# Kernel tuning notes

Measured on AMD Instinct MI355X. Metric: run time of the kernel, lower is better.

## Reference

```python
import jax, jax.numpy as jnp
import numpy as np

N_NODES = 100000
N_EDGES = 1600000
NUM_GRAPHS = 128
F_IN = 64
HID = 64


def setup_inputs() -> dict:
    key = jax.random.key(0)
    ks = jax.random.split(key, 10)
    x = jax.random.normal(ks[0], (N_NODES, F_IN), dtype=jnp.float32)
    edge_index = jax.random.randint(ks[1], (2, N_EDGES), 0, N_NODES, dtype=jnp.int64)
    batch = jnp.sort(jax.random.randint(ks[2], (N_NODES,), 0, NUM_GRAPHS, dtype=jnp.int64))
    def glorot(k, shape):
        lim = float(np.sqrt(6.0 / (shape[0] + shape[1])))
        return jax.random.uniform(k, shape, dtype=jnp.float32, minval=-lim, maxval=lim)
    return {
        "x": x,
        "edge_index": edge_index,
        "batch": batch,
        "W1": glorot(ks[3], (F_IN, HID)), "b1": jnp.zeros((HID,), jnp.float32),
        "W2": glorot(ks[4], (HID, HID)), "b2": jnp.zeros((HID,), jnp.float32),
        "W3": glorot(ks[5], (HID, HID)), "b3": jnp.zeros((HID,), jnp.float32),
        "fc1_w": glorot(ks[6], (HID, 10)), "fc1_b": jnp.zeros((10,), jnp.float32),
        "fc2_w": glorot(ks[7], (10, 1)), "fc2_b": jnp.zeros((1,), jnp.float32),
    }


def reference(x, edge_index, batch, W1, b1, W2, b2, W3, b3, fc1_w, fc1_b, fc2_w, fc2_b):
    n = x.shape[0]
    # GCN normalization with self-loops (PyG gcn_norm): deg over dst incl. self-loop
    loop = jnp.arange(n, dtype=edge_index.dtype)
    src = jnp.concatenate([edge_index[0], loop])
    dst = jnp.concatenate([edge_index[1], loop])
    deg = jax.ops.segment_sum(jnp.ones_like(dst, dtype=x.dtype), dst, num_segments=n)
    dinv = jnp.where(deg > 0, jax.lax.rsqrt(deg), 0.0)
    norm = (dinv[src] * dinv[dst])[:, None]  # [E+N, 1]

    def gcn_conv(h, W, b):
        h = h @ W                      # dense linear transform
        msg = h[src] * norm            # gather + degree normalize
        agg = jax.ops.segment_sum(msg, dst, num_segments=n)  # scatter-add
        return agg + b

    h = jax.nn.relu(gcn_conv(x, W1, b1))
    h = jax.nn.relu(gcn_conv(h, W2, b2))
    h = jax.nn.relu(gcn_conv(h, W3, b3))

    # global mean pool over graphs
    sums = jax.ops.segment_sum(h, batch, num_segments=NUM_GRAPHS)
    counts = jax.ops.segment_sum(jnp.ones((n,), h.dtype), batch, num_segments=NUM_GRAPHS)
    pooled = sums / jnp.maximum(counts, 1.0)[:, None]  # [NUM_GRAPHS, HID]

    out = jax.nn.relu(pooled @ fc1_w + fc1_b)
    return out @ fc2_w + fc2_b  # [NUM_GRAPHS, 1]
```

## Files before the change

### kernel.cpp

```cpp
#include <hip/hip_runtime.h>
#include <hip/hip_fp16.h>

#define N_NODES   100000
#define N_EDGES   1600000
#define NUM_GRAPHS 128
#define HID       64

#define NB   512
#define NPB  196
#define NBU  511
#define CPE  3125
#define CSR_TOT (N_EDGES + N_NODES)


__global__ void k_zero(int* __restrict__ p, int n) {
  int i = blockIdx.x * blockDim.x + threadIdx.x;
  if (i < n) p[i] = 0;
}

__global__ void k_f2h(const float* __restrict__ in, __half* __restrict__ out, int n4) {
  int i = blockIdx.x * blockDim.x + threadIdx.x;
  if (i >= n4) return;
  float4 v = ((const float4*)in)[i];
  ((__half2*)out)[2 * i]     = __floats2half2_rn(v.x, v.y);
  ((__half2*)out)[2 * i + 1] = __floats2half2_rn(v.z, v.w);
}

__global__ __launch_bounds__(256) void k_b1a(const int* __restrict__ dst, int* __restrict__ H) {
  __shared__ int hist[NB];
  int w = blockIdx.x, t = threadIdx.x;
  for (int b = t; b < NB; b += 256) hist[b] = 0;
  __syncthreads();
  int e0 = w * CPE;
  for (int i = t; i < CPE; i += 256)
    atomicAdd(&hist[dst[e0 + i] / NPB], 1);
  __syncthreads();
  for (int b = t; b < NB; b += 256) H[w * NB + b] = hist[b];
}

__global__ __launch_bounds__(256) void k_colsum(const int* __restrict__ H, int* __restrict__ S) {
  __shared__ int red[256];
  int b = blockIdx.x, t = threadIdx.x;
  red[t] = H[t * NB + b] + H[(t + 256) * NB + b];
  __syncthreads();
  for (int d = 128; d > 0; d >>= 1) { if (t < d) red[t] += red[t + d]; __syncthreads(); }
  if (t == 0) S[b] = red[0];
}

__global__ __launch_bounds__(512) void k_rowscan(const int* __restrict__ H,
                                                 const int* __restrict__ S,
                                                 int* __restrict__ bstart,
                                                 int* __restrict__ OT) {
  __shared__ int sb[NB];
  __shared__ int sc[NB];
  int b = blockIdx.x, t = threadIdx.x;
  int sv = S[t];
  sb[t] = sv; __syncthreads();
  for (int d = 1; d < NB; d <<= 1) {
    int x = (t >= d) ? sb[t - d] : 0; __syncthreads();
    sb[t] += x; __syncthreads();
  }
  int bst = sb[b] - S[b];
  if (t == 0) bstart[b] = bst;
  if (b == NB - 1 && t == 0) bstart[NB] = sb[NB - 1];
  int v = H[t * NB + b];
  sc[t] = v; __syncthreads();
  for (int d = 1; d < NB; d <<= 1) {
    int x = (t >= d) ? sc[t - d] : 0; __syncthreads();
    sc[t] += x; __syncthreads();
  }
  OT[b * NB + t] = bst + sc[t] - v;
}

__global__ __launch_bounds__(256) void k_b1b(const int* __restrict__ src,
                                             const int* __restrict__ dst,
                                             const int* __restrict__ OT,
                                             int2* __restrict__ staged) {
  __shared__ int pos[NB];
  int w = blockIdx.x, t = threadIdx.x;
  for (int b = t; b < NB; b += 256) pos[b] = OT[b * NB + w];
  __syncthreads();
  int e0 = w * CPE;
  for (int i = t; i < CPE; i += 256) {
    int s = src[e0 + i], d = dst[e0 + i];
    int p = atomicAdd(&pos[d / NPB], 1);
    staged[p] = make_int2(s, d);
  }
}

__global__ __launch_bounds__(256) void k_b2a(const int2* __restrict__ staged,
                                             const int* __restrict__ bstart,
                                             int* __restrict__ row_off,
                                             float* __restrict__ dinv) {
  __shared__ int cnt[256];
  __shared__ int sc[256];
  int b = blockIdx.x, t = threadIdx.x;
  int nloc = min(NPB, N_NODES - b * NPB);
  cnt[t] = 0;
  __syncthreads();
  int s0 = bstart[b], s1 = bstart[b + 1];
  for (int i = s0 + t; i < s1; i += 256)
    atomicAdd(&cnt[staged[i].y - b * NPB], 1);
  __syncthreads();
  int v = (t < nloc) ? cnt[t] + 1 : 0;
  sc[t] = v; __syncthreads();
  for (int d = 1; d < 256; d <<= 1) {
    int x = (t >= d) ? sc[t - d] : 0; __syncthreads();
    sc[t] += x; __syncthreads();
  }
  if (t < nloc) {
    int g = b * NPB + t;
    row_off[g] = bstart[b] + b * NPB + (sc[t] - v);
    dinv[g] = rsqrtf((float)(cnt[t] + 1));
  }
  if (b == 0 && t == 0) row_off[N_NODES] = CSR_TOT;
}

__global__ __launch_bounds__(256) void k_b2b(const int2* __restrict__ staged,
                                             const int* __restrict__ bstart,
                                             const int* __restrict__ row_off,
                                             const float* __restrict__ dinv,
                                             int2* __restrict__ csr) {
  __shared__ int pos[NPB];
  __shared__ float dl[NPB];
  int b = blockIdx.x, t = threadIdx.x;
  int nloc = min(NPB, N_NODES - b * NPB);
  if (t < nloc) {
    int g = b * NPB + t;
    int ro = row_off[g];
    float dv = dinv[g];
    csr[ro] = make_int2(g, __float_as_int(dv * dv));
    pos[t] = ro + 1;
    dl[t] = dv;
  }
  __syncthreads();
  int s0 = bstart[b], s1 = bstart[b + 1];
  for (int i = s0 + t; i < s1; i += 256) {
    int2 e = staged[i];
    int l = e.y - b * NPB;
    int p = atomicAdd(&pos[l], 1);
    csr[p] = make_int2(e.x, __float_as_int(dl[l] * dinv[e.x]));
  }
}


__global__ __launch_bounds__(256) void k_gemm(const __half* __restrict__ A,
                                              const float* __restrict__ W,
                                              __half* __restrict__ C) {
  __shared__ float sW[64 * 64];
  __shared__ float sA[64][65];
  int tid = threadIdx.x;
  #pragma unroll
  for (int i = tid; i < 1024; i += 256)
    ((float4*)sW)[i] = ((const float4*)W)[i];
  int row0 = blockIdx.x * 64;
  #pragma unroll
  for (int i = tid; i < 1024; i += 256) {
    int r = i >> 4, c4 = (i & 15) << 2;
    int row = row0 + r;
    if (row < N_NODES) {
      __half2 a = *(const __half2*)(A + (size_t)row * 64 + c4);
      __half2 b = *(const __half2*)(A + (size_t)row * 64 + c4 + 2);
      float2 fa = __half22float2(a), fb = __half22float2(b);
      sA[r][c4 + 0] = fa.x; sA[r][c4 + 1] = fa.y;
      sA[r][c4 + 2] = fb.x; sA[r][c4 + 3] = fb.y;
    } else {
      sA[r][c4 + 0] = 0.f; sA[r][c4 + 1] = 0.f; sA[r][c4 + 2] = 0.f; sA[r][c4 + 3] = 0.f;
    }
  }
  __syncthreads();
  int tr = (tid >> 4) << 2;
  int tc = (tid & 15) << 2;
  float acc[4][4];
  #pragma unroll
  for (int i = 0; i < 4; ++i)
    #pragma unroll
    for (int j = 0; j < 4; ++j) acc[i][j] = 0.f;
  #pragma unroll 8
  for (int k = 0; k < 64; ++k) {
    float4 w = *(const float4*)&sW[k * 64 + tc];
    float a0 = sA[tr + 0][k], a1 = sA[tr + 1][k], a2 = sA[tr + 2][k], a3 = sA[tr + 3][k];
    acc[0][0] += a0 * w.x; acc[0][1] += a0 * w.y; acc[0][2] += a0 * w.z; acc[0][3] += a0 * w.w;
    acc[1][0] += a1 * w.x; acc[1][1] += a1 * w.y; acc[1][2] += a1 * w.z; acc[1][3] += a1 * w.w;
    acc[2][0] += a2 * w.x; acc[2][1] += a2 * w.y; acc[2][2] += a2 * w.z; acc[2][3] += a2 * w.w;
    acc[3][0] += a3 * w.x; acc[3][1] += a3 * w.y; acc[3][2] += a3 * w.z; acc[3][3] += a3 * w.w;
  }
  #pragma unroll
  for (int i = 0; i < 4; ++i) {
    int row = row0 + tr + i;
    if (row < N_NODES) {
      *(__half2*)(C + (size_t)row * 64 + tc)     = __floats2half2_rn(acc[i][0], acc[i][1]);
      *(__half2*)(C + (size_t)row * 64 + tc + 2) = __floats2half2_rn(acc[i][2], acc[i][3]);
    }
  }
}


__global__ __launch_bounds__(256) void k_agg(const __half2* __restrict__ hw2,
                                             const int* __restrict__ row_off,
                                             const int2* __restrict__ csr,
                                             const float2* __restrict__ bias2,
                                             __half2* __restrict__ out2) {
  int tid = threadIdx.x;
  int half_id = tid >> 5;
  int f = tid & 31;
  int v = blockIdx.x * 8 + half_id;
  if (v >= N_NODES) return;
  int o = row_off[v], e = row_off[v + 1];
  float accx = 0.f, accy = 0.f;
  int i = o;
  for (; i + 4 <= e; i += 4) {
    int2 p0 = csr[i + 0];
    int2 p1 = csr[i + 1];
    int2 p2 = csr[i + 2];
    int2 p3 = csr[i + 3];
    float2 h0 = __half22float2(hw2[(size_t)p0.x * 32 + f]);
    float2 h1 = __half22float2(hw2[(size_t)p1.x * 32 + f]);
    float2 h2 = __half22float2(hw2[(size_t)p2.x * 32 + f]);
    float2 h3 = __half22float2(hw2[(size_t)p3.x * 32 + f]);
    float n0 = __int_as_float(p0.y), n1 = __int_as_float(p1.y);
    float n2 = __int_as_float(p2.y), n3 = __int_as_float(p3.y);
    accx += n0 * h0.x; accy += n0 * h0.y;
    accx += n1 * h1.x; accy += n1 * h1.y;
    accx += n2 * h2.x; accy += n2 * h2.y;
    accx += n3 * h3.x; accy += n3 * h3.y;
  }
  for (; i < e; ++i) {
    int2 p = csr[i];
    float2 h = __half22float2(hw2[(size_t)p.x * 32 + f]);
    float n = __int_as_float(p.y);
    accx += n * h.x; accy += n * h.y;
  }
  float2 b = bias2[f];
  out2[(size_t)v * 32 + f] =
      __floats2half2_rn(fmaxf(accx + b.x, 0.f), fmaxf(accy + b.y, 0.f));
}


#define POOL_CHUNK 32

__global__ __launch_bounds__(256) void k_pool(const __half* __restrict__ h,
                                              const int* __restrict__ batch,
                                              float* __restrict__ pooled,
                                              int* __restrict__ pcnt) {
  int wid = threadIdx.x >> 6, lane = threadIdx.x & 63;
  int w = blockIdx.x * (blockDim.x >> 6) + wid;
  int v0 = w * POOL_CHUNK;
  if (v0 >= N_NODES) return;
  int vend = min(v0 + POOL_CHUNK, N_NODES);
  int g = batch[v0];
  float acc = 0.0f;
  int cnt = 0;
  for (int v = v0; v < vend; ++v) {
    int gv = batch[v];
    if (gv != g) {
      atomicAdd(&pooled[g * HID + lane], acc);
      if (lane == 0) atomicAdd(&pcnt[g], cnt);
      g = gv; acc = 0.0f; cnt = 0;
    }
    acc += __half2float(h[(size_t)v * HID + lane]);
    ++cnt;
  }
  atomicAdd(&pooled[g * HID + lane], acc);
  if (lane == 0) atomicAdd(&pcnt[g], cnt);
}

__global__ void k_mlp(const float* __restrict__ pooled, const int* __restrict__ pcnt,
                      const float* __restrict__ fc1w, const float* __restrict__ fc1b,
                      const float* __restrict__ fc2w, const float* __restrict__ fc2b,
                      float* __restrict__ out) {
  int g = threadIdx.x;
  if (g >= NUM_GRAPHS) return;
  float inv = 1.0f / fmaxf((float)pcnt[g], 1.0f);
  float hid[10];
  #pragma unroll
  for (int j = 0; j < 10; ++j) hid[j] = fc1b[j];
  for (int k = 0; k < HID; ++k) {
    float p = pooled[g * HID + k] * inv;
    #pragma unroll
    for (int j = 0; j < 10; ++j) hid[j] += p * fc1w[k * 10 + j];
  }
  float o = fc2b[0];
  #pragma unroll
  for (int j = 0; j < 10; ++j) o += fmaxf(hid[j], 0.0f) * fc2w[j];
  out[g] = o;
}


extern "C" void kernel_launch(void* const* d_in, const int* in_sizes, int n_in,
                              void* d_out, int out_size, void* d_ws, size_t ws_size,
                              hipStream_t stream) {
  const float* x    = (const float*)d_in[0];
  const int*   ei   = (const int*)d_in[1];
  const int*   batch= (const int*)d_in[2];
  const float* W1   = (const float*)d_in[3];
  const float* b1   = (const float*)d_in[4];
  const float* W2   = (const float*)d_in[5];
  const float* b2   = (const float*)d_in[6];
  const float* W3   = (const float*)d_in[7];
  const float* b3   = (const float*)d_in[8];
  const float* fc1w = (const float*)d_in[9];
  const float* fc1b = (const float*)d_in[10];
  const float* fc2w = (const float*)d_in[11];
  const float* fc2b = (const float*)d_in[12];

  const int* e_src = ei;
  const int* e_dst = ei + N_EDGES;

  char* ws = (char*)d_ws;
  auto alignup = [](size_t o, size_t a) { return (o + a - 1) / a * a; };
  size_t off = 0;
  int*   H      = (int*)(ws + off);  off += (size_t)NB * NB * 4;
  int*   pcnt   = (int*)(ws + off);  off += 128 * 4;
  float* pooled = (float*)(ws + off); off += 8192 * 4;
  const int ZERO_N = NB * NB + 128 + 8192;
  int*   S      = (int*)(ws + off);  off += NB * 4;
  int*   bstart = (int*)(ws + off);  off += (NB + 1) * 4;  off = alignup(off, 256);
  int*   OT     = (int*)(ws + off);  off += (size_t)NB * NB * 4;          off = alignup(off, 256);
  int*   row_off= (int*)(ws + off);  off += (size_t)(N_NODES + 1) * 4;    off = alignup(off, 256);
  float* dinv   = (float*)(ws + off); off += (size_t)N_NODES * 4;         off = alignup(off, 256);
  int2*  csr    = (int2*)(ws + off); off += (size_t)CSR_TOT * 8;          off = alignup(off, 256);
  __half* xh    = (__half*)(ws + off); off += (size_t)N_NODES * HID * 2;  off = alignup(off, 256);
  __half* h_a   = (__half*)(ws + off); off += (size_t)N_NODES * HID * 2;  off = alignup(off, 256);
  int2*  staged = (int2*)(ws + off);
  __half* h_b   = (__half*)(ws + off); off += (size_t)N_EDGES * 8;
  (void)ws_size; (void)in_sizes; (void)n_in; (void)out_size;

  const int TB = 256;
  k_zero   <<<(ZERO_N + TB - 1) / TB, TB, 0, stream>>>(H, ZERO_N);
  k_f2h    <<<(N_NODES * HID / 4 + TB - 1) / TB, TB, 0, stream>>>(x, xh, N_NODES * HID / 4);
  k_b1a    <<<NB, TB, 0, stream>>>(e_dst, H);
  k_colsum <<<NB, TB, 0, stream>>>(H, S);
  k_rowscan<<<NB, 512, 0, stream>>>(H, S, bstart, OT);
  k_b1b    <<<NB, TB, 0, stream>>>(e_src, e_dst, OT, staged);
  k_b2a    <<<NBU, TB, 0, stream>>>(staged, bstart, row_off, dinv);
  k_b2b    <<<NBU, TB, 0, stream>>>(staged, bstart, row_off, dinv, csr);

  const int GEMM_GRID = (N_NODES + 63) / 64;
  const int AGG_GRID  = (N_NODES + 7) / 8;

  k_gemm<<<GEMM_GRID, TB, 0, stream>>>(xh, W1, h_a);
  k_agg <<<AGG_GRID, TB, 0, stream>>>((const __half2*)h_a, row_off, csr,
                                      (const float2*)b1, (__half2*)h_b);
  k_gemm<<<GEMM_GRID, TB, 0, stream>>>(h_b, W2, h_a);
  k_agg <<<AGG_GRID, TB, 0, stream>>>((const __half2*)h_a, row_off, csr,
                                      (const float2*)b2, (__half2*)h_b);
  k_gemm<<<GEMM_GRID, TB, 0, stream>>>(h_b, W3, h_a);
  k_agg <<<AGG_GRID, TB, 0, stream>>>((const __half2*)h_a, row_off, csr,
                                      (const float2*)b3, (__half2*)h_b);

  const int POOL_GRID = ((N_NODES + POOL_CHUNK - 1) / POOL_CHUNK + 3) / 4;
  k_pool<<<POOL_GRID, TB, 0, stream>>>(h_b, batch, pooled, pcnt);
  k_mlp <<<1, 128, 0, stream>>>(pooled, pcnt, fc1w, fc1b, fc2w, fc2b, (float*)d_out);
}
```

Baseline: 287.7 us.

## Sort nodes by degree and aggregate with 8 lanes per node using 16-byte loads

```diff
diff --git a/kernel.cpp b/kernel.cpp
--- a/kernel.cpp
+++ b/kernel.cpp
@@ -144,6 +144,55 @@
 }
 
 
+__global__ __launch_bounds__(256) void k_dhist(const int* __restrict__ row_off,
+                                               int* __restrict__ dbins) {
+  __shared__ int h[256];
+  int t = threadIdx.x;
+  h[t] = 0;
+  __syncthreads();
+  int v = blockIdx.x * 256 + t;
+  if (v < N_NODES) {
+    int deg = min(row_off[v + 1] - row_off[v], 255);
+    atomicAdd(&h[deg], 1);
+  }
+  __syncthreads();
+  if (h[t] > 0) atomicAdd(&dbins[t], h[t]);
+}
+
+__global__ __launch_bounds__(256) void k_dscan(const int* __restrict__ dbins,
+                                               int* __restrict__ dpos) {
+  __shared__ int sc[256];
+  int t = threadIdx.x;
+  int v = dbins[t];
+  sc[t] = v; __syncthreads();
+  for (int d = 1; d < 256; d <<= 1) {
+    int x = (t >= d) ? sc[t - d] : 0; __syncthreads();
+    sc[t] += x; __syncthreads();
+  }
+  dpos[t] = sc[t] - v;
+}
+
+__global__ __launch_bounds__(256) void k_dperm(const int* __restrict__ row_off,
+                                               int* __restrict__ dpos,
+                                               int* __restrict__ perm) {
+  __shared__ int cnt[256];
+  __shared__ int sbase[256];
+  int t = threadIdx.x;
+  cnt[t] = 0;
+  __syncthreads();
+  int v = blockIdx.x * 256 + t;
+  int bin = 0, rank = 0;
+  if (v < N_NODES) {
+    bin = min(row_off[v + 1] - row_off[v], 255);
+    rank = atomicAdd(&cnt[bin], 1);
+  }
+  __syncthreads();
+  if (cnt[t] > 0) sbase[t] = atomicAdd(&dpos[t], cnt[t]);
+  __syncthreads();
+  if (v < N_NODES) perm[sbase[bin] + rank] = v;
+}
+
+
 __global__ __launch_bounds__(256) void k_gemm(const __half* __restrict__ A,
                                               const float* __restrict__ W,
                                               __half* __restrict__ C) {
@@ -196,44 +245,80 @@
 }
 
 
-__global__ __launch_bounds__(256) void k_agg(const __half2* __restrict__ hw2,
+__device__ __forceinline__ void fma8(float* acc, float n, uint4 h) {
+  __half2 u0 = *(__half2*)&h.x, u1 = *(__half2*)&h.y;
+  __half2 u2 = *(__half2*)&h.z, u3 = *(__half2*)&h.w;
+  float2 f0 = __half22float2(u0), f1 = __half22float2(u1);
+  float2 f2 = __half22float2(u2), f3 = __half22float2(u3);
+  acc[0] = fmaf(n, f0.x, acc[0]); acc[1] = fmaf(n, f0.y, acc[1]);
+  acc[2] = fmaf(n, f1.x, acc[2]); acc[3] = fmaf(n, f1.y, acc[3]);
+  acc[4] = fmaf(n, f2.x, acc[4]); acc[5] = fmaf(n, f2.y, acc[5]);
+  acc[6] = fmaf(n, f3.x, acc[6]); acc[7] = fmaf(n, f3.y, acc[7]);
+}
+
+__global__ __launch_bounds__(256) void k_agg(const __half* __restrict__ hw,
                                              const int* __restrict__ row_off,
                                              const int2* __restrict__ csr,
-                                             const float2* __restrict__ bias2,
-                                             __half2* __restrict__ out2) {
+                                             const int* __restrict__ perm,
+                                             const float* __restrict__ bias,
+                                             __half* __restrict__ out) {
   int tid = threadIdx.x;
-  int half_id = tid >> 5;
-  int f = tid & 31;
-  int v = blockIdx.x * 8 + half_id;
-  if (v >= N_NODES) return;
-  int o = row_off[v], e = row_off[v + 1];
-  float accx = 0.f, accy = 0.f;
-  int i = o;
-  for (; i + 4 <= e; i += 4) {
-    int2 p0 = csr[i + 0];
-    int2 p1 = csr[i + 1];
-    int2 p2 = csr[i + 2];
-    int2 p3 = csr[i + 3];
-    float2 h0 = __half22float2(hw2[(size_t)p0.x * 32 + f]);
-    float2 h1 = __half22float2(hw2[(size_t)p1.x * 32 + f]);
-    float2 h2 = __half22float2(hw2[(size_t)p2.x * 32 + f]);
-    float2 h3 = __half22float2(hw2[(size_t)p3.x * 32 + f]);
-    float n0 = __int_as_float(p0.y), n1 = __int_as_float(p1.y);
-    float n2 = __int_as_float(p2.y), n3 = __int_as_float(p3.y);
-    accx += n0 * h0.x; accy += n0 * h0.y;
-    accx += n1 * h1.x; accy += n1 * h1.y;
-    accx += n2 * h2.x; accy += n2 * h2.y;
-    accx += n3 * h3.x; accy += n3 * h3.y;
-  }
-  for (; i < e; ++i) {
-    int2 p = csr[i];
-    float2 h = __half22float2(hw2[(size_t)p.x * 32 + f]);
-    float n = __int_as_float(p.y);
-    accx += n * h.x; accy += n * h.y;
-  }
-  float2 b = bias2[f];
-  out2[(size_t)v * 32 + f] =
-      __floats2half2_rn(fmaxf(accx + b.x, 0.f), fmaxf(accy + b.y, 0.f));
+  int lane = tid & 63;
+  int sg = lane >> 3;
+  int k = lane & 7;
+  int slot = (blockIdx.x * 4 + (tid >> 6)) * 8 + sg;
+  int v = -1, o = 0, d = 1;
+  if (slot < N_NODES) {
+    v = perm[slot];
+    o = row_off[v];
+    d = row_off[v + 1] - o;
+  }
+  int m = d;
+  m = max(m, __shfl_xor(m, 8));
+  m = max(m, __shfl_xor(m, 16));
+  m = max(m, __shfl_xor(m, 32));
+  float acc[8];
+  #pragma unroll
+  for (int j = 0; j < 8; ++j) acc[j] = 0.f;
+  const __half* hk = hw + k * 8;
+  int dm1 = d - 1;
+  int i = 0;
+  for (; i + 4 <= m; i += 4) {
+    int2 p0 = csr[o + min(i + 0, dm1)];
+    int2 p1 = csr[o + min(i + 1, dm1)];
+    int2 p2 = csr[o + min(i + 2, dm1)];
+    int2 p3 = csr[o + min(i + 3, dm1)];
+    uint4 h0 = *(const uint4*)(hk + (size_t)p0.x * 64);
+    uint4 h1 = *(const uint4*)(hk + (size_t)p1.x * 64);
+    uint4 h2 = *(const uint4*)(hk + (size_t)p2.x * 64);
+    uint4 h3 = *(const uint4*)(hk + (size_t)p3.x * 64);
+    float n0 = (i + 0 < d) ? __int_as_float(p0.y) : 0.f;
+    float n1 = (i + 1 < d) ? __int_as_float(p1.y) : 0.f;
+    float n2 = (i + 2 < d) ? __int_as_float(p2.y) : 0.f;
+    float n3 = (i + 3 < d) ? __int_as_float(p3.y) : 0.f;
+    fma8(acc, n0, h0);
+    fma8(acc, n1, h1);
+    fma8(acc, n2, h2);
+    fma8(acc, n3, h3);
+  }
+  for (; i < m; ++i) {
+    int2 p = csr[o + min(i, dm1)];
+    uint4 h = *(const uint4*)(hk + (size_t)p.x * 64);
+    float n = (i < d) ? __int_as_float(p.y) : 0.f;
+    fma8(acc, n, h);
+  }
+  if (v >= 0) {
+    float4 b0 = *(const float4*)(bias + k * 8);
+    float4 b1 = *(const float4*)(bias + k * 8 + 4);
+    __half2 q0 = __floats2half2_rn(fmaxf(acc[0] + b0.x, 0.f), fmaxf(acc[1] + b0.y, 0.f));
+    __half2 q1 = __floats2half2_rn(fmaxf(acc[2] + b0.z, 0.f), fmaxf(acc[3] + b0.w, 0.f));
+    __half2 q2 = __floats2half2_rn(fmaxf(acc[4] + b1.x, 0.f), fmaxf(acc[5] + b1.y, 0.f));
+    __half2 q3 = __floats2half2_rn(fmaxf(acc[6] + b1.z, 0.f), fmaxf(acc[7] + b1.w, 0.f));
+    uint4 r;
+    r.x = *(unsigned int*)&q0; r.y = *(unsigned int*)&q1;
+    r.z = *(unsigned int*)&q2; r.w = *(unsigned int*)&q3;
+    *(uint4*)(out + (size_t)v * HID + k * 8) = r;
+  }
 }
 
 
@@ -313,12 +398,15 @@
   int*   H      = (int*)(ws + off);  off += (size_t)NB * NB * 4;
   int*   pcnt   = (int*)(ws + off);  off += 128 * 4;
   float* pooled = (float*)(ws + off); off += 8192 * 4;
-  const int ZERO_N = NB * NB + 128 + 8192;
+  int*   dbins  = (int*)(ws + off);  off += 256 * 4;
+  const int ZERO_N = NB * NB + 128 + 8192 + 256;
   int*   S      = (int*)(ws + off);  off += NB * 4;
-  int*   bstart = (int*)(ws + off);  off += (NB + 1) * 4;  off = alignup(off, 256);
+  int*   bstart = (int*)(ws + off);  off += (NB + 1) * 4;
+  int*   dpos   = (int*)(ws + off);  off += 256 * 4;       off = alignup(off, 256);
   int*   OT     = (int*)(ws + off);  off += (size_t)NB * NB * 4;          off = alignup(off, 256);
   int*   row_off= (int*)(ws + off);  off += (size_t)(N_NODES + 1) * 4;    off = alignup(off, 256);
   float* dinv   = (float*)(ws + off); off += (size_t)N_NODES * 4;         off = alignup(off, 256);
+  int*   perm   = (int*)(ws + off);  off += (size_t)N_NODES * 4;          off = alignup(off, 256);
   int2*  csr    = (int2*)(ws + off); off += (size_t)CSR_TOT * 8;          off = alignup(off, 256);
   __half* xh    = (__half*)(ws + off); off += (size_t)N_NODES * HID * 2;  off = alignup(off, 256);
   __half* h_a   = (__half*)(ws + off); off += (size_t)N_NODES * HID * 2;  off = alignup(off, 256);
@@ -327,6 +415,7 @@
   (void)ws_size; (void)in_sizes; (void)n_in; (void)out_size;
 
   const int TB = 256;
+  const int NGRID = (N_NODES + TB - 1) / TB;
   k_zero   <<<(ZERO_N + TB - 1) / TB, TB, 0, stream>>>(H, ZERO_N);
   k_f2h    <<<(N_NODES * HID / 4 + TB - 1) / TB, TB, 0, stream>>>(x, xh, N_NODES * HID / 4);
   k_b1a    <<<NB, TB, 0, stream>>>(e_dst, H);
@@ -335,19 +424,19 @@
   k_b1b    <<<NB, TB, 0, stream>>>(e_src, e_dst, OT, staged);
   k_b2a    <<<NBU, TB, 0, stream>>>(staged, bstart, row_off, dinv);
   k_b2b    <<<NBU, TB, 0, stream>>>(staged, bstart, row_off, dinv, csr);
+  k_dhist  <<<NGRID, TB, 0, stream>>>(row_off, dbins);
+  k_dscan  <<<1, TB, 0, stream>>>(dbins, dpos);
+  k_dperm  <<<NGRID, TB, 0, stream>>>(row_off, dpos, perm);
 
   const int GEMM_GRID = (N_NODES + 63) / 64;
-  const int AGG_GRID  = (N_NODES + 7) / 8;
+  const int AGG_GRID  = (N_NODES + 31) / 32;
 
   k_gemm<<<GEMM_GRID, TB, 0, stream>>>(xh, W1, h_a);
-  k_agg <<<AGG_GRID, TB, 0, stream>>>((const __half2*)h_a, row_off, csr,
-                                      (const float2*)b1, (__half2*)h_b);
+  k_agg <<<AGG_GRID, TB, 0, stream>>>(h_a, row_off, csr, perm, b1, h_b);
   k_gemm<<<GEMM_GRID, TB, 0, stream>>>(h_b, W2, h_a);
-  k_agg <<<AGG_GRID, TB, 0, stream>>>((const __half2*)h_a, row_off, csr,
-                                      (const float2*)b2, (__half2*)h_b);
+  k_agg <<<AGG_GRID, TB, 0, stream>>>(h_a, row_off, csr, perm, b2, h_b);
   k_gemm<<<GEMM_GRID, TB, 0, stream>>>(h_b, W3, h_a);
-  k_agg <<<AGG_GRID, TB, 0, stream>>>((const __half2*)h_a, row_off, csr,
-                                      (const float2*)b3, (__half2*)h_b);
+  k_agg <<<AGG_GRID, TB, 0, stream>>>(h_a, row_off, csr, perm, b3, h_b);
 
   const int POOL_GRID = ((N_NODES + POOL_CHUNK - 1) / POOL_CHUNK + 3) / 4;
   k_pool<<<POOL_GRID, TB, 0, stream>>>(h_b, batch, pooled, pcnt);
```

Result: faster. 275.4 us (-4.3%).
